# Performance work log

Measured on AMD Instinct MI355X. Metric: run time of the kernel, lower is better.

## Reference

```python
import jax, jax.numpy as jnp
import numpy as np

B, C, F, H, W = 8, 16, 256, 112, 112   # batch, cells/image, channels, height, width
NB = 3                                  # tgt_shape = (3, 3) adaptive pool bins


def setup_inputs() -> dict:
    key = jax.random.key(0)
    kf, ky, kx, kry, krx, kn = jax.random.split(key, 6)
    feature_maps = jax.random.normal(kf, (B, F, H, W), jnp.float32)
    N = B * C
    # random rectangular cell blobs with bernoulli interior holes + guaranteed core
    cy = jax.random.randint(ky, (N, 1, 1), 20, H - 20)
    cx = jax.random.randint(kx, (N, 1, 1), 20, W - 20)
    ry = jax.random.randint(kry, (N, 1, 1), 5, 18)
    rx = jax.random.randint(krx, (N, 1, 1), 5, 18)
    yy = jnp.arange(H)[None, :, None]
    xx = jnp.arange(W)[None, None, :]
    rect = (jnp.abs(yy - cy) <= ry) & (jnp.abs(xx - cx) <= rx)
    noise = jax.random.bernoulli(kn, 0.8, (N, H, W))
    core = (jnp.abs(yy - cy) <= 2) & (jnp.abs(xx - cx) <= 2)
    cell_masks = rect & (noise | core)            # [N, H, W] bool, each nonempty
    cell_counts = jnp.full((B,), C, jnp.int32)    # fixed cells per image
    return {"feature_maps": feature_maps, "cell_masks": cell_masks,
            "cell_counts": cell_counts}


def _bin_membership(lo, hi, length):
    # adaptive-pool bin i covers [lo + floor(i*sz/NB), lo + ceil((i+1)*sz/NB))
    i = jnp.arange(NB)
    sz = (hi - lo)[..., None]                      # [B, C, 1]
    start = lo[..., None] + (i * sz) // NB         # [B, C, NB]
    end = lo[..., None] + ((i + 1) * sz + NB - 1) // NB
    pos = jnp.arange(length)
    return (pos >= start[..., None]) & (pos < end[..., None])  # [B, C, NB, L]


def reference(feature_maps, cell_masks, cell_counts):
    Bv, Fv, Hv, Wv = feature_maps.shape
    Cv = cell_masks.shape[0] // Bv
    masks = cell_masks.reshape(Bv, Cv, Hv, Wv)
    # tight bbox per cell (first/last True row and column, exclusive end)
    rows = masks.any(-1)                            # [B, C, H]
    cols = masks.any(-2)                            # [B, C, W]
    y0 = jnp.argmax(rows, -1)
    y1 = Hv - jnp.argmax(rows[..., ::-1], -1)
    x0 = jnp.argmax(cols, -1)
    x1 = Wv - jnp.argmax(cols[..., ::-1], -1)
    ymem = _bin_membership(y0, y1, Hv)              # [B, C, NB, H]
    xmem = _bin_membership(x0, x1, Wv)              # [B, C, NB, W]
    neg = jnp.finfo(feature_maps.dtype).min
    feat = feature_maps[:, None]                    # [B, 1, F, H, W]
    m = masks[:, :, None]                           # [B, C, 1, H, W]
    pooled = []
    for i in range(NB):
        ym = ymem[:, :, i][:, :, None, :, None]     # [B, C, 1, H, 1]
        for j in range(NB):
            xm = xmem[:, :, j][:, :, None, None, :]  # [B, C, 1, 1, W]
            inbin = ym & xm
            # inside bin & mask -> feature; inside bin & ~mask -> 0 (zeroed crop);
            # outside bin -> -inf (excluded from max)
            v = jnp.where(inbin & m, feat, jnp.where(inbin, 0.0, neg))
            pooled.append(v.max((-1, -2)))          # [B, C, F]
    out = jnp.stack(pooled, -1)                     # [B, C, F, 9], index = i*NB + j
    # matches torch pooled.view(-1): flatten order f*9 + i*3 + j
    return out.reshape(Bv * Cv, Fv * NB * NB)
```

## Files before the change

kernel.cpp:

```cpp
#include <hip/hip_runtime.h>
#include <float.h>

#define B_  8
#define C_  16
#define N_  (B_*C_)
#define F_  256
#define H_  112
#define W_  112
#define HW_ (H_*W_)
#define NB_ 3

#define FPAR 2
#define FSEQ 2
#define FPW  (FPAR*FSEQ)
#define WPB  4
#define FPB  (FPW*WPB)
#define LMS  64


__global__ __launch_bounds__(256) void bbox_kernel(const int4* __restrict__ mask4,
                                                   int* __restrict__ bb) {
    int n = blockIdx.x, t = threadIdx.x;
    const int4* m = mask4 + (size_t)n * (HW_ / 4);
    int ymin = 1 << 20, ymax = -1, xmin = 1 << 20, xmax = -1;
    for (int i = t; i < HW_ / 4; i += 256) {
        int4 v = m[i];
        int y = i / 28;
        int xb = (i - y * 28) * 4;
        if (v.x | v.y | v.z | v.w) { ymin = min(ymin, y); ymax = max(ymax, y); }
        if (v.x) { xmin = min(xmin, xb);     xmax = max(xmax, xb);     }
        if (v.y) { xmin = min(xmin, xb + 1); xmax = max(xmax, xb + 1); }
        if (v.z) { xmin = min(xmin, xb + 2); xmax = max(xmax, xb + 2); }
        if (v.w) { xmin = min(xmin, xb + 3); xmax = max(xmax, xb + 3); }
    }
    #pragma unroll
    for (int off = 32; off; off >>= 1) {
        ymin = min(ymin, __shfl_xor(ymin, off));
        ymax = max(ymax, __shfl_xor(ymax, off));
        xmin = min(xmin, __shfl_xor(xmin, off));
        xmax = max(xmax, __shfl_xor(xmax, off));
    }
    __shared__ int red[4][4];
    int wave = t >> 6;
    if ((t & 63) == 0) {
        red[wave][0] = ymin; red[wave][1] = ymax;
        red[wave][2] = xmin; red[wave][3] = xmax;
    }
    __syncthreads();
    if (t == 0) {
        for (int w = 1; w < 4; ++w) {
            ymin = min(ymin, red[w][0]); ymax = max(ymax, red[w][1]);
            xmin = min(xmin, red[w][2]); xmax = max(xmax, red[w][3]);
        }
        int y0 = ymin, y1 = ymax + 1, x0 = xmin, x1 = xmax + 1;
        int* o = bb + n * 16;
        o[0] = y0; o[1] = y1; o[2] = x0; o[3] = x1;
        int szy = y1 - y0, szx = x1 - x0;
        for (int i = 0; i < NB_; ++i) {
            o[4+i]  = y0 + (i*szy)/NB_;
            o[7+i]  = y0 + ((i+1)*szy + NB_-1)/NB_;
            o[10+i] = x0 + (i*szx)/NB_;
            o[13+i] = x0 + ((i+1)*szx + NB_-1)/NB_;
        }
    }
}

__global__ __launch_bounds__(256) void pool_kernel(
        const float* __restrict__ feat, const int* __restrict__ mask,
        const int* __restrict__ bb, float* __restrict__ out) {
    int n = blockIdx.x;
    int b = n >> 4;
    const int* o = bb + n * 16;
    int y0 = o[0], x0 = o[2];
    int bh = o[1] - y0, bw = o[3] - x0;
    int x0a = x0 & ~3;
    int woff = x0 - x0a;
    int x1 = x0 + bw;

    __shared__ float lm[37 * LMS];
    for (int idx = threadIdx.x; idx < bh * LMS; idx += 256) {
        int dy = idx >> 6, xo = idx & 63;
        int gx = x0a + xo;
        float v = 0.0f;
        if (gx >= x0 && gx < x1)
            v = mask[(size_t)n * HW_ + (size_t)(y0 + dy) * W_ + gx] ? 1.0f : 0.0f;
        lm[idx] = v;
    }
    __syncthreads();

    int lane = threadIdx.x & 63, wave = threadIdx.x >> 6;
    int xq = lane & 15, rg = lane >> 4;
    int xq4  = (4 * xq < woff + bw) ? 4 * xq : 0;
    int f0 = blockIdx.y * FPB + wave * FPW;

    int ys0 = o[4], ys1 = o[5], ys2 = o[6];
    int ye0 = o[7], ye1 = o[8], ye2 = o[9];
    int xs0 = o[10], xs1 = o[11], xs2 = o[12];
    int xe0 = o[13], xe1 = o[14], xe2 = o[15];

    int ntiles = (bh + 3) >> 2;
    int bhm1 = bh - 1;
    const float* gbase = feat + (size_t)(b * F_) * HW_ + (size_t)y0 * W_ + x0a + xq4;

    for (int fs = 0; fs < FSEQ; ++fs) {
        int f = f0 + fs * FPAR;
        const float* gp0 = gbase + (size_t)f * HW_;
        const float* gp1 = gp0 + HW_;

        float acc[3][4][FPAR];
        #pragma unroll
        for (int i = 0; i < 3; ++i)
            #pragma unroll
            for (int s = 0; s < 4; ++s)
                #pragma unroll
                for (int pp = 0; pp < FPAR; ++pp) acc[i][s][pp] = -FLT_MAX;

        int dy0 = min(rg, bhm1);
        float4 cur0 = *(const float4*)(gp0 + dy0 * W_);
        float4 cur1 = *(const float4*)(gp1 + dy0 * W_);

        for (int t = 0; t < ntiles; ++t) {
            int tn = (t + 1 < ntiles) ? t + 1 : t;
            int dyn = min(4 * tn + rg, bhm1);
            float4 nxt0 = *(const float4*)(gp0 + dyn * W_);
            float4 nxt1 = *(const float4*)(gp1 + dyn * W_);

            int dyc = min(4 * t + rg, bhm1);
            float4 mv = *(const float4*)(&lm[dyc * LMS + 4 * xq]);
            int y = y0 + dyc;
            bool in0 = (y >= ys0) & (y < ye0);
            bool in1 = (y >= ys1) & (y < ye1);
            bool in2 = (y >= ys2) & (y < ye2);

            float v0[4] = {mv.x * cur0.x, mv.y * cur0.y, mv.z * cur0.z, mv.w * cur0.w};
            float v1[4] = {mv.x * cur1.x, mv.y * cur1.y, mv.z * cur1.z, mv.w * cur1.w};
            #pragma unroll
            for (int s = 0; s < 4; ++s) {
                if (in0) { acc[0][s][0] = fmaxf(acc[0][s][0], v0[s]);
                           acc[0][s][1] = fmaxf(acc[0][s][1], v1[s]); }
                if (in1) { acc[1][s][0] = fmaxf(acc[1][s][0], v0[s]);
                           acc[1][s][1] = fmaxf(acc[1][s][1], v1[s]); }
                if (in2) { acc[2][s][0] = fmaxf(acc[2][s][0], v0[s]);
                           acc[2][s][1] = fmaxf(acc[2][s][1], v1[s]); }
            }
            cur0 = nxt0; cur1 = nxt1;
        }

        int xg = x0a + 4 * xq;
        #pragma unroll
        for (int pp = 0; pp < FPAR; ++pp) {
            float part[9];
            #pragma unroll
            for (int i = 0; i < 3; ++i) {
                #pragma unroll
                for (int s = 0; s < 4; ++s) {
                    int xx = xg + s;
                    float a = acc[i][s][pp];
                    float p0 = (xx >= xs0 && xx < xe0) ? a : -FLT_MAX;
                    float p1 = (xx >= xs1 && xx < xe1) ? a : -FLT_MAX;
                    float p2 = (xx >= xs2 && xx < xe2) ? a : -FLT_MAX;
                    if (s == 0) { part[i*3+0] = p0; part[i*3+1] = p1; part[i*3+2] = p2; }
                    else {
                        part[i*3+0] = fmaxf(part[i*3+0], p0);
                        part[i*3+1] = fmaxf(part[i*3+1], p1);
                        part[i*3+2] = fmaxf(part[i*3+2], p2);
                    }
                }
            }
            #pragma unroll
            for (int off = 32; off; off >>= 1)
                #pragma unroll
                for (int q = 0; q < 9; ++q)
                    part[q] = fmaxf(part[q], __shfl_xor(part[q], off));
            float st = part[0];
            #pragma unroll
            for (int q = 1; q < 9; ++q) st = (lane == q) ? part[q] : st;
            if (lane < 9)
                out[(size_t)(n * F_ + f + pp) * 9 + lane] = st;
        }
    }
}

extern "C" void kernel_launch(void* const* d_in, const int* in_sizes, int n_in,
                              void* d_out, int out_size, void* d_ws, size_t ws_size,
                              hipStream_t stream) {
    const float* feat = (const float*)d_in[0];
    const int*   mask = (const int*)d_in[1];
    int* bb = (int*)d_ws;

    bbox_kernel<<<N_, 256, 0, stream>>>((const int4*)mask, bb);
    dim3 grid(N_, F_ / FPB);
    pool_kernel<<<grid, 256, 0, stream>>>(feat, mask, bb, (float*)d_out);
}
```

Before: 184.8 us.

## Restructure pool kernel into per-row-bin fully unrolled loads with width-adaptive lane mapping

Rewrites the pooling kernel so each row bin is handled by a fully unrolled fixed-trip loop over clamped rows. This replaces the tiled sweep with per-row bin predicates. Lane-to-column grouping is chosen at runtime (8 or 16 column quads) based on bbox width, so narrow cells use more rows per wave. Blocks shrink to 128 threads with one feature pair per wave, giving four times as many blocks. The mask staging into shared memory now uses int4 vector loads. The cost is more blocks and repeated mask staging per block, plus redundant loads of clamped rows.

After: 259.4 us. 40.4% more time.

```diff
diff --git a/kernel.cpp b/kernel.cpp
--- a/kernel.cpp
+++ b/kernel.cpp
@@ -11,10 +11,8 @@
 #define NB_ 3
 
 #define FPAR 2
-#define FSEQ 2
-#define FPW  (FPAR*FSEQ)
-#define WPB  4
-#define FPB  (FPW*WPB)
+#define WPB  2
+#define FPB  (FPAR*WPB)
 #define LMS  64
 
 
@@ -65,7 +63,84 @@
     }
 }
 
-__global__ __launch_bounds__(256) void pool_kernel(
+template<int XGL>
+__device__ __forceinline__ void pool_body(
+        const float* __restrict__ gp0, const float* __restrict__ gp1,
+        const float* __restrict__ lm, const int* __restrict__ o,
+        float* __restrict__ out, int n, int f0,
+        int y0, int x0a, int wbw, int lane)
+{
+    constexpr int XG  = 1 << XGL;
+    constexpr int RT  = 64 >> XGL;
+    constexpr int TPB = 16 / RT;
+    int xq = lane & (XG - 1);
+    int rg = lane >> XGL;
+    int xq4 = (4 * xq < wbw) ? 4 * xq : 0;
+
+    const float* p0 = gp0 + xq4;
+    const float* p1 = gp1 + xq4;
+
+    float acc[3][4][FPAR];
+    #pragma unroll
+    for (int i = 0; i < 3; ++i)
+        #pragma unroll
+        for (int s = 0; s < 4; ++s)
+            #pragma unroll
+            for (int pp = 0; pp < FPAR; ++pp) acc[i][s][pp] = -FLT_MAX;
+
+    #pragma unroll
+    for (int i = 0; i < 3; ++i) {
+        int ys = o[4 + i], yem1 = o[7 + i] - 1;
+        #pragma unroll
+        for (int t = 0; t < TPB; ++t) {
+            int row = ys + RT * t + rg;
+            row = min(row, yem1);
+            int dy = row - y0;
+            float4 mv = *(const float4*)(lm + dy * LMS + 4 * xq);
+            float4 c0 = *(const float4*)(p0 + dy * W_);
+            float4 c1 = *(const float4*)(p1 + dy * W_);
+            float v0[4] = {mv.x*c0.x, mv.y*c0.y, mv.z*c0.z, mv.w*c0.w};
+            float v1[4] = {mv.x*c1.x, mv.y*c1.y, mv.z*c1.z, mv.w*c1.w};
+            #pragma unroll
+            for (int s = 0; s < 4; ++s) {
+                acc[i][s][0] = fmaxf(acc[i][s][0], v0[s]);
+                acc[i][s][1] = fmaxf(acc[i][s][1], v1[s]);
+            }
+        }
+    }
+
+    int xg = x0a + 4 * xq;
+    #pragma unroll
+    for (int pp = 0; pp < FPAR; ++pp) {
+        float part[9];
+        #pragma unroll
+        for (int j = 0; j < 3; ++j) {
+            int xs = o[10 + j], xe = o[13 + j];
+            #pragma unroll
+            for (int i = 0; i < 3; ++i) {
+                float r = -FLT_MAX;
+                #pragma unroll
+                for (int s = 0; s < 4; ++s) {
+                    int xx = xg + s;
+                    float lim = (xx >= xs && xx < xe) ? FLT_MAX : -FLT_MAX;
+                    r = fmaxf(r, fminf(acc[i][s][pp], lim));
+                }
+                part[i * 3 + j] = r;
+            }
+        }
+        #pragma unroll
+        for (int off = 32; off; off >>= 1)
+            #pragma unroll
+            for (int q = 0; q < 9; ++q)
+                part[q] = fmaxf(part[q], __shfl_xor(part[q], off));
+        float st = part[0];
+        #pragma unroll
+        for (int q = 1; q < 9; ++q) st = (lane == q) ? part[q] : st;
+        if (lane < 9) out[(size_t)(n * F_ + f0 + pp) * 9 + lane] = st;
+    }
+}
+
+__global__ __launch_bounds__(128, 8) void pool_kernel(
         const float* __restrict__ feat, const int* __restrict__ mask,
         const int* __restrict__ bb, float* __restrict__ out) {
     int n = blockIdx.x;
@@ -74,111 +149,34 @@
     int y0 = o[0], x0 = o[2];
     int bh = o[1] - y0, bw = o[3] - x0;
     int x0a = x0 & ~3;
-    int woff = x0 - x0a;
+    int wbw = (x0 - x0a) + bw;
     int x1 = x0 + bw;
 
     __shared__ float lm[37 * LMS];
-    for (int idx = threadIdx.x; idx < bh * LMS; idx += 256) {
-        int dy = idx >> 6, xo = idx & 63;
-        int gx = x0a + xo;
-        float v = 0.0f;
-        if (gx >= x0 && gx < x1)
-            v = mask[(size_t)n * HW_ + (size_t)(y0 + dy) * W_ + gx] ? 1.0f : 0.0f;
-        lm[idx] = v;
+    {
+        const int* mrow = mask + (size_t)n * HW_ + (size_t)y0 * W_ + x0a;
+        int tot = bh * (LMS / 4);
+        for (int idx = threadIdx.x; idx < tot; idx += 128) {
+            int dy = idx >> 4, g = idx & 15;
+            int gx = x0a + 4 * g;
+            int4 m4 = *(const int4*)(mrow + (size_t)dy * W_ + 4 * g);
+            float4 v;
+            v.x = (m4.x && gx     >= x0 && gx     < x1) ? 1.f : 0.f;
+            v.y = (m4.y && gx + 1 >= x0 && gx + 1 < x1) ? 1.f : 0.f;
+            v.z = (m4.z && gx + 2 >= x0 && gx + 2 < x1) ? 1.f : 0.f;
+            v.w = (m4.w && gx + 3 >= x0 && gx + 3 < x1) ? 1.f : 0.f;
+            *(float4*)(&lm[dy * LMS + 4 * g]) = v;
+        }
     }
     __syncthreads();
 
     int lane = threadIdx.x & 63, wave = threadIdx.x >> 6;
-    int xq = lane & 15, rg = lane >> 4;
-    int xq4  = (4 * xq < woff + bw) ? 4 * xq : 0;
-    int f0 = blockIdx.y * FPB + wave * FPW;
+    int f0 = blockIdx.y * FPB + wave * FPAR;
+    const float* gp0 = feat + (size_t)(b * F_ + f0) * HW_ + (size_t)y0 * W_ + x0a;
+    const float* gp1 = gp0 + HW_;
 
-    int ys0 = o[4], ys1 = o[5], ys2 = o[6];
-    int ye0 = o[7], ye1 = o[8], ye2 = o[9];
-    int xs0 = o[10], xs1 = o[11], xs2 = o[12];
-    int xe0 = o[13], xe1 = o[14], xe2 = o[15];
-
-    int ntiles = (bh + 3) >> 2;
-    int bhm1 = bh - 1;
-    const float* gbase = feat + (size_t)(b * F_) * HW_ + (size_t)y0 * W_ + x0a + xq4;
-
-    for (int fs = 0; fs < FSEQ; ++fs) {
-        int f = f0 + fs * FPAR;
-        const float* gp0 = gbase + (size_t)f * HW_;
-        const float* gp1 = gp0 + HW_;
-
-        float acc[3][4][FPAR];
-        #pragma unroll
-        for (int i = 0; i < 3; ++i)
-            #pragma unroll
-            for (int s = 0; s < 4; ++s)
-                #pragma unroll
-                for (int pp = 0; pp < FPAR; ++pp) acc[i][s][pp] = -FLT_MAX;
-
-        int dy0 = min(rg, bhm1);
-        float4 cur0 = *(const float4*)(gp0 + dy0 * W_);
-        float4 cur1 = *(const float4*)(gp1 + dy0 * W_);
-
-        for (int t = 0; t < ntiles; ++t) {
-            int tn = (t + 1 < ntiles) ? t + 1 : t;
-            int dyn = min(4 * tn + rg, bhm1);
-            float4 nxt0 = *(const float4*)(gp0 + dyn * W_);
-            float4 nxt1 = *(const float4*)(gp1 + dyn * W_);
-
-            int dyc = min(4 * t + rg, bhm1);
-            float4 mv = *(const float4*)(&lm[dyc * LMS + 4 * xq]);
-            int y = y0 + dyc;
-            bool in0 = (y >= ys0) & (y < ye0);
-            bool in1 = (y >= ys1) & (y < ye1);
-            bool in2 = (y >= ys2) & (y < ye2);
-
-            float v0[4] = {mv.x * cur0.x, mv.y * cur0.y, mv.z * cur0.z, mv.w * cur0.w};
-            float v1[4] = {mv.x * cur1.x, mv.y * cur1.y, mv.z * cur1.z, mv.w * cur1.w};
-            #pragma unroll
-            for (int s = 0; s < 4; ++s) {
-                if (in0) { acc[0][s][0] = fmaxf(acc[0][s][0], v0[s]);
-                           acc[0][s][1] = fmaxf(acc[0][s][1], v1[s]); }
-                if (in1) { acc[1][s][0] = fmaxf(acc[1][s][0], v0[s]);
-                           acc[1][s][1] = fmaxf(acc[1][s][1], v1[s]); }
-                if (in2) { acc[2][s][0] = fmaxf(acc[2][s][0], v0[s]);
-                           acc[2][s][1] = fmaxf(acc[2][s][1], v1[s]); }
-            }
-            cur0 = nxt0; cur1 = nxt1;
-        }
-
-        int xg = x0a + 4 * xq;
-        #pragma unroll
-        for (int pp = 0; pp < FPAR; ++pp) {
-            float part[9];
-            #pragma unroll
-            for (int i = 0; i < 3; ++i) {
-                #pragma unroll
-                for (int s = 0; s < 4; ++s) {
-                    int xx = xg + s;
-                    float a = acc[i][s][pp];
-                    float p0 = (xx >= xs0 && xx < xe0) ? a : -FLT_MAX;
-                    float p1 = (xx >= xs1 && xx < xe1) ? a : -FLT_MAX;
-                    float p2 = (xx >= xs2 && xx < xe2) ? a : -FLT_MAX;
-                    if (s == 0) { part[i*3+0] = p0; part[i*3+1] = p1; part[i*3+2] = p2; }
-                    else {
-                        part[i*3+0] = fmaxf(part[i*3+0], p0);
-                        part[i*3+1] = fmaxf(part[i*3+1], p1);
-                        part[i*3+2] = fmaxf(part[i*3+2], p2);
-                    }
-                }
-            }
-            #pragma unroll
-            for (int off = 32; off; off >>= 1)
-                #pragma unroll
-                for (int q = 0; q < 9; ++q)
-                    part[q] = fmaxf(part[q], __shfl_xor(part[q], off));
-            float st = part[0];
-            #pragma unroll
-            for (int q = 1; q < 9; ++q) st = (lane == q) ? part[q] : st;
-            if (lane < 9)
-                out[(size_t)(n * F_ + f + pp) * 9 + lane] = st;
-        }
-    }
+    if (wbw <= 32) pool_body<3>(gp0, gp1, lm, o, out, n, f0, y0, x0a, wbw, lane);
+    else           pool_body<4>(gp0, gp1, lm, o, out, n, f0, y0, x0a, wbw, lane);
 }
 
 extern "C" void kernel_launch(void* const* d_in, const int* in_sizes, int n_in,
@@ -190,5 +188,5 @@
 
     bbox_kernel<<<N_, 256, 0, stream>>>((const int4*)mask, bb);
     dim3 grid(N_, F_ / FPB);
-    pool_kernel<<<grid, 256, 0, stream>>>(feat, mask, bb, (float*)d_out);
+    pool_kernel<<<grid, 128, 0, stream>>>(feat, mask, bb, (float*)d_out);
 }
```
